# Kernel optimization log

Measured on AMD Instinct MI355X. Metric: run time of the kernel, lower is better.

Reference implementation:

```python
import jax, jax.numpy as jnp
import numpy as np


def setup_inputs() -> dict:
    key = jax.random.key(0)
    k1, k2, k3 = jax.random.split(key, 3)
    B, T, C = 4, 2048, 1024
    x = jax.random.normal(k1, (B, T, C), dtype=jnp.float32)
    # Linear weights stored as (in, out) so y = x @ W + b
    w_attn = jax.random.normal(k2, (C, 3 * C), dtype=jnp.float32) * (1.0 / np.sqrt(C))
    b_attn = jnp.zeros((3 * C,), dtype=jnp.float32)
    w_proj = jax.random.normal(k3, (C, C), dtype=jnp.float32) * (1.0 / np.sqrt(C))
    b_proj = jnp.zeros((C,), dtype=jnp.float32)
    return {"x": x, "w_attn": w_attn, "b_attn": b_attn, "w_proj": w_proj, "b_proj": b_proj}


def reference(x, w_attn, b_attn, w_proj, b_proj):
    B, T, C = x.shape
    n_head = 16
    hd = C // n_head  # head dim = 64
    qkv = x @ w_attn + b_attn  # [B, T, 3C]
    q, k, v = jnp.split(qkv, 3, axis=-1)
    # [B, H, T, hd]
    q = q.reshape(B, T, n_head, hd).transpose(0, 2, 1, 3)
    k = k.reshape(B, T, n_head, hd).transpose(0, 2, 1, 3)
    v = v.reshape(B, T, n_head, hd).transpose(0, 2, 1, 3)
    scale = 1.0 / np.sqrt(hd).astype(np.float32)
    att = jnp.einsum("bhqd,bhkd->bhqk", q, k) * scale  # [B, H, T, T]
    causal = jnp.tril(jnp.ones((T, T), dtype=bool))
    att = jnp.where(causal[None, None], att, jnp.float32(-jnp.inf))
    att = jax.nn.softmax(att, axis=-1)
    y = jnp.einsum("bhqk,bhkd->bhqd", att, v)  # [B, H, T, hd]
    y = y.transpose(0, 2, 1, 3).reshape(B, T, C)
    return y @ w_proj + b_proj
```

## Files before the change

kernel.cpp:

```cpp
#include <hip/hip_runtime.h>

typedef __attribute__((ext_vector_type(8))) short short8;
typedef __attribute__((ext_vector_type(4))) float f32x4;
typedef __attribute__((ext_vector_type(16))) float f32x16;
typedef unsigned short u16;
typedef unsigned int u32;

__device__ __forceinline__ float bf2f(u16 u) {
    union { u32 i; float f; } x;
    x.i = ((u32)u) << 16;
    return x.f;
}

__device__ __forceinline__ u16 f2bf(float f) {
    union { float f; u32 i; } x;
    x.f = f;
    u32 r = x.i + 0x7fffu + ((x.i >> 16) & 1u);
    return (u16)(r >> 16);
}

__device__ __forceinline__ u32 cvt_pk_bf16(float lo, float hi) {
    u32 d;
    asm("v_cvt_pk_bf16_f32 %0, %1, %2" : "=v"(d) : "v"(lo), "v"(hi));
    return d;
}

__device__ __forceinline__ void gload_lds16(const u16* g, u16* l) {
    __builtin_amdgcn_global_load_lds(
        (const __attribute__((address_space(1))) void*)g,
        (__attribute__((address_space(3))) void*)l, 16, 0, 0);
}

__device__ __forceinline__ void pswap(u32& a, u32& b) {
#if __has_builtin(__builtin_amdgcn_permlane32_swap)
    auto r = __builtin_amdgcn_permlane32_swap(a, b, false, false);
    a = r[0];
    b = r[1];
#else
    const int l = (int)(threadIdx.x & 63);
    const u32 ax = __shfl(a, l ^ 32);
    const u32 bx = __shfl(b, l ^ 32);
    a = (l < 32) ? a : bx;
    b = (l < 32) ? ax : b;
#endif
}

#if __has_builtin(__builtin_amdgcn_exp2f)
#define EXP2F(x) __builtin_amdgcn_exp2f(x)
#else
#define EXP2F(x) exp2f(x)
#endif

#define K_SCALE 0.18033688f

__global__ __launch_bounds__(256) void prep_kernel(const float* __restrict__ x,
                                                   u16* __restrict__ xb,
                                                   const float* __restrict__ w_attn,
                                                   u16* __restrict__ wTa) {
    __shared__ float tile[32][33];
    const int tid = threadIdx.x;
    if (blockIdx.x < 4096) {
        const long i = ((long)blockIdx.x * 256 + tid) * 8;
        f32x4 v0 = *(const f32x4*)(x + i);
        f32x4 v1 = *(const f32x4*)(x + i + 4);
        short8 o;
#pragma unroll
        for (int j = 0; j < 4; ++j) o[j] = (short)f2bf(v0[j]);
#pragma unroll
        for (int j = 0; j < 4; ++j) o[4 + j] = (short)f2bf(v1[j]);
        *(short8*)(xb + i) = o;
    } else {
        const int bid = blockIdx.x - 4096;
        const int nb = (bid % 96) * 32, kb = (bid / 96) * 32;
        const int tx = tid & 31, ty = tid >> 5;
#pragma unroll
        for (int i = 0; i < 32; i += 8)
            tile[ty + i][tx] = w_attn[(long)(kb + ty + i) * 3072 + nb + tx];
        __syncthreads();
#pragma unroll
        for (int i = 0; i < 32; i += 8)
            wTa[(long)(nb + ty + i) * 1024 + kb + tx] = f2bf(tile[tx][ty + i]);
    }
}

__global__ __launch_bounds__(256) void transpose_v(const u16* __restrict__ qkv,
                                                   u16* __restrict__ vT) {
    __shared__ u16 tile[32][33];
    const int tb = blockIdx.x * 32;
    const int db = blockIdx.y * 32;
    const int bh = blockIdx.z;
    const int b = bh >> 4, h = bh & 15;
    const int tx = threadIdx.x, ty = threadIdx.y;
#pragma unroll
    for (int i = 0; i < 32; i += 8)
        tile[ty + i][tx] = qkv[((long)b * 2048 + tb + ty + i) * 3072 + 2048 + h * 64 + db + tx];
    __syncthreads();
#pragma unroll
    for (int i = 0; i < 32; i += 8)
        vT[((long)bh * 64 + db + ty + i) * 2048 + tb + tx] = tile[tx][ty + i];
}

#define G1_STAGE(KOFF, SLOT)                                                  \
    gload_lds16(Ag + (KOFF), &As[(SLOT)*4096 + wbase]);                       \
    gload_lds16(Ag + (KOFF) + (long)16 * lda, &As[(SLOT)*4096 + wbase + 512]);\
    gload_lds16(Bg + (KOFF), &Bs[(SLOT)*4096 + wbase]);                       \
    gload_lds16(Bg + (KOFF) + (long)16 * K, &Bs[(SLOT)*4096 + wbase + 512]);

#define G1_COMPUTE(SLOT)                                                      \
    {                                                                         \
        short8 af[4], bf[4];                                                  \
        _Pragma("unroll")                                                     \
        for (int mt = 0; mt < 4; ++mt)                                        \
            af[mt] = *(const short8*)&As[(SLOT)*4096 + (wm + mt*16 + L)*32 + quad*8]; \
        _Pragma("unroll")                                                     \
        for (int nt = 0; nt < 4; ++nt)                                        \
            bf[nt] = *(const short8*)&Bs[(SLOT)*4096 + (wn + nt*16 + L)*32 + quad*8]; \
        _Pragma("unroll")                                                     \
        for (int mt = 0; mt < 4; ++mt)                                        \
            _Pragma("unroll")                                                 \
            for (int nt = 0; nt < 4; ++nt)                                    \
                acc[mt][nt] = __builtin_amdgcn_mfma_f32_16x16x32_bf16(        \
                    af[mt], bf[nt], acc[mt][nt], 0, 0, 0);                    \
    }

__global__ __launch_bounds__(256, 3) void gemm_bf16_bt(
    const u16* __restrict__ A, int lda, const u16* __restrict__ BT,
    const float* __restrict__ bias, u16* __restrict__ C,
    int M, int N, int K) {
    __shared__ __align__(16) u16 As[3 * 128 * 32];
    __shared__ __align__(16) u16 Bs[3 * 128 * 32];
    const int tid = threadIdx.x;
    const int wv = tid >> 6, lane = tid & 63, quad = lane >> 4, L = lane & 15;
    const int wm = (wv >> 1) * 64, wn = (wv & 1) * 64;
    const long m0 = (long)blockIdx.y * 128;
    const long n0 = (long)blockIdx.x * 128;

    const u16* Ag = A + (m0 + wv * 32 + (lane >> 2)) * (long)lda + (lane & 3) * 8;
    const u16* Bg = BT + (n0 + wv * 32 + (lane >> 2)) * (long)K + (lane & 3) * 8;
    const int wbase = wv * 1024;

    f32x4 zero4 = {0.f, 0.f, 0.f, 0.f};
    f32x4 acc[4][4];
#pragma unroll
    for (int i = 0; i < 4; ++i)
#pragma unroll
        for (int j = 0; j < 4; ++j) acc[i][j] = zero4;

    G1_STAGE(0, 0);
    G1_STAGE(32, 1);

    int slot = 0, s2 = 2;
    for (int kb = 0; kb + 64 < K; kb += 32) {
        asm volatile("s_waitcnt vmcnt(4)" ::: "memory");
        __builtin_amdgcn_s_barrier();
        G1_STAGE(kb + 64, s2);
        G1_COMPUTE(slot);
        slot = (slot + 1 == 3) ? 0 : slot + 1;
        s2 = (s2 + 1 == 3) ? 0 : s2 + 1;
    }
    asm volatile("s_waitcnt vmcnt(4)" ::: "memory");
    __builtin_amdgcn_s_barrier();
    G1_COMPUTE(slot);
    slot = (slot + 1 == 3) ? 0 : slot + 1;
    asm volatile("s_waitcnt vmcnt(0)" ::: "memory");
    __builtin_amdgcn_s_barrier();
    G1_COMPUTE(slot);

#pragma unroll
    for (int nt = 0; nt < 4; ++nt) {
        const long col = n0 + wn + nt * 16 + L;
        const float bv = bias[col];
        const float scl = (col >= 1024 && col < 2048) ? K_SCALE : 1.0f;
#pragma unroll
        for (int mt = 0; mt < 4; ++mt)
#pragma unroll
            for (int r = 0; r < 4; ++r) {
                const long row = m0 + wm + mt * 16 + quad * 4 + r;
                C[row * N + col] = f2bf((acc[mt][nt][r] + bv) * scl);
            }
    }
}

__global__ __launch_bounds__(256, 2) void gemm_bf16_bn(
    const u16* __restrict__ A, int lda, const float* __restrict__ B,
    const float* __restrict__ bias, float* __restrict__ C,
    int M, int N, int K) {
    __shared__ __align__(16) u16 As[128 * 32];
    __shared__ __align__(16) u16 Bs[128 * 32];
    const int tid = threadIdx.x;
    const int wv = tid >> 6, lane = tid & 63, quad = lane >> 4, L = lane & 15;
    const int wm = (wv >> 1) * 64, wn = (wv & 1) * 64;
    const long m0 = (long)blockIdx.y * 128;
    const long n0 = (long)blockIdx.x * 128;

    const u16* Ag = A + (m0 + wv * 32 + (lane >> 2)) * (long)lda + (lane & 3) * 8;
    u16* AsW = &As[wv * 32 * 32];

    f32x4 zero4 = {0.f, 0.f, 0.f, 0.f};
    f32x4 acc[4][4];
#pragma unroll
    for (int i = 0; i < 4; ++i)
#pragma unroll
        for (int j = 0; j < 4; ++j) acc[i][j] = zero4;

    for (int kb = 0; kb < K; kb += 32) {
        short8 p[2];
#pragma unroll
        for (int i = 0; i < 2; ++i) {
            const int c = tid + i * 256;
            const int n = c >> 2, k8 = (c & 3) * 8;
            const float* bp = B + (long)(kb + k8) * N + n0 + n;
            float f[8];
#pragma unroll
            for (int j = 0; j < 8; ++j) f[j] = bp[(long)j * N];
            union { u32 d[4]; short8 v; } u;
#pragma unroll
            for (int j = 0; j < 4; ++j) u.d[j] = cvt_pk_bf16(f[2 * j], f[2 * j + 1]);
            p[i] = u.v;
        }
        __syncthreads();
        gload_lds16(Ag + kb, AsW);
        gload_lds16(Ag + kb + (long)16 * lda, AsW + 512);
        *(short8*)(&Bs[tid * 8]) = p[0];
        *(short8*)(&Bs[(tid + 256) * 8]) = p[1];
        __syncthreads();

        short8 af[4], bf[4];
#pragma unroll
        for (int mt = 0; mt < 4; ++mt)
            af[mt] = *(const short8*)&As[(wm + mt * 16 + L) * 32 + quad * 8];
#pragma unroll
        for (int nt = 0; nt < 4; ++nt)
            bf[nt] = *(const short8*)&Bs[(wn + nt * 16 + L) * 32 + quad * 8];
#pragma unroll
        for (int mt = 0; mt < 4; ++mt)
#pragma unroll
            for (int nt = 0; nt < 4; ++nt)
                acc[mt][nt] = __builtin_amdgcn_mfma_f32_16x16x32_bf16(
                    af[mt], bf[nt], acc[mt][nt], 0, 0, 0);
    }

#pragma unroll
    for (int nt = 0; nt < 4; ++nt) {
        const long col = n0 + wn + nt * 16 + L;
        const float bv = bias[col];
#pragma unroll
        for (int mt = 0; mt < 4; ++mt)
#pragma unroll
            for (int r = 0; r < 4; ++r) {
                const long row = m0 + wm + mt * 16 + quad * 4 + r;
                C[row * N + col] = acc[mt][nt][r] + bv;
            }
    }
}

#define AT_T 2048

__global__ __launch_bounds__(256) void attn_kernel(u16* __restrict__ qkv,
                                                   const u16* __restrict__ vT) {
    __shared__ u16 Kt[2][64 * 72];
    __shared__ u16 Vt[2][64 * 72];
    const int tid = threadIdx.x;
    const int wv = tid >> 6, lane = tid & 63;
    const int hi = lane >> 5, cc = lane & 31;
    const int bh = blockIdx.x;
    const int b = bh >> 4, h = bh & 15;
    const long rowbase = (long)b * AT_T;
    const long cbase = (long)h * 64;

    const int srow = tid >> 3, sc = tid & 7;
    const u16* Kg = qkv + (rowbase + srow) * 3072 + 1024 + cbase + sc * 8;
    const u16* Vg = vT + ((long)bh * 64 + srow) * 2048 + sc * 8;
    const int kLo = srow * 72 + sc * 8, kHi = (srow + 32) * 72 + sc * 8;

    short8 ones;
#pragma unroll
    for (int j = 0; j < 8; ++j) ones[j] = (cc == 0) ? (short)0x3F80 : (short)0;

    f32x16 z16;
#pragma unroll
    for (int r = 0; r < 16; ++r) z16[r] = 0.f;

    for (int pass = 0; pass < 2; ++pass) {
        const int qt = (pass == 0) ? (15 - (int)blockIdx.y) : (int)blockIdx.y;
        const int qw = qt * 128 + wv * 32;
        const int nkb = 2 * qt + 2;

        short8 qf[4];
#pragma unroll
        for (int ks = 0; ks < 4; ++ks)
            qf[ks] = *(const short8*)&qkv[(rowbase + qw + cc) * 3072 + cbase + ks * 16 + hi * 8];

        f32x16 accO0, accO1, accL;
#pragma unroll
        for (int r = 0; r < 16; ++r) { accO0[r] = 0.f; accO1[r] = 0.f; accL[r] = 0.f; }

        {
            *(short8*)&Kt[0][kLo] = *(const short8*)Kg;
            *(short8*)&Kt[0][kHi] = *(const short8*)(Kg + (long)32 * 3072);
            *(short8*)&Vt[0][kLo] = *(const short8*)Vg;
            *(short8*)&Vt[0][kHi] = *(const short8*)(Vg + (long)32 * 2048);
        }
        __syncthreads();

        int p = 0;
        for (int kb = 0; kb < nkb; ++kb) {
            const int k0 = kb * 64;
            const bool more = (kb + 1) < nkb;
            short8 kn0, kn1, vn0, vn1;
            if (more) {
                kn0 = *(const short8*)(Kg + (long)(k0 + 64) * 3072);
                kn1 = *(const short8*)(Kg + (long)(k0 + 96) * 3072);
                vn0 = *(const short8*)(Vg + k0 + 64);
                vn1 = *(const short8*)(Vg + (long)32 * 2048 + k0 + 64);
            }

#pragma unroll
            for (int hh = 0; hh < 2; ++hh) {
                const int kh = k0 + 32 * hh;
                if (kh <= qw) {
                    f32x16 s;
                    {
                        short8 kf = *(const short8*)&Kt[p][(32 * hh + cc) * 72 + hi * 8];
                        s = __builtin_amdgcn_mfma_f32_32x32x16_bf16(kf, qf[0], z16, 0, 0, 0);
                    }
#pragma unroll
                    for (int ks = 1; ks < 4; ++ks) {
                        short8 kf = *(const short8*)&Kt[p][(32 * hh + cc) * 72 + ks * 16 + hi * 8];
                        s = __builtin_amdgcn_mfma_f32_32x32x16_bf16(kf, qf[ks], s, 0, 0, 0);
                    }
                    float pe[16];
                    if (kh == qw) {
#pragma unroll
                        for (int r = 0; r < 16; ++r) {
                            const int key = (r & 3) + 8 * (r >> 2) + 4 * hi;
                            const float e = EXP2F(s[r]);
                            pe[r] = (key <= cc) ? e : 0.f;
                        }
                    } else {
#pragma unroll
                        for (int r = 0; r < 16; ++r) pe[r] = EXP2F(s[r]);
                    }

                    short8 pa[2];
#pragma unroll
                    for (int ks = 0; ks < 2; ++ks) {
                        u32 wA = cvt_pk_bf16(pe[8 * ks + 0], pe[8 * ks + 1]);
                        u32 wB = cvt_pk_bf16(pe[8 * ks + 2], pe[8 * ks + 3]);
                        u32 wC = cvt_pk_bf16(pe[8 * ks + 4], pe[8 * ks + 5]);
                        u32 wD = cvt_pk_bf16(pe[8 * ks + 6], pe[8 * ks + 7]);
                        pswap(wA, wC);
                        pswap(wB, wD);
                        union { u32 d[4]; short8 v; } u;
                        u.d[0] = wA; u.d[1] = wB; u.d[2] = wC; u.d[3] = wD;
                        pa[ks] = u.v;
                    }

                    accL = __builtin_amdgcn_mfma_f32_32x32x16_bf16(pa[0], ones, accL, 0, 0, 0);
                    accL = __builtin_amdgcn_mfma_f32_32x32x16_bf16(pa[1], ones, accL, 0, 0, 0);
#pragma unroll
                    for (int ks = 0; ks < 2; ++ks) {
                        short8 vf0 = *(const short8*)&Vt[p][cc * 72 + 32 * hh + ks * 16 + hi * 8];
                        short8 vf1 = *(const short8*)&Vt[p][(32 + cc) * 72 + 32 * hh + ks * 16 + hi * 8];
                        accO0 = __builtin_amdgcn_mfma_f32_32x32x16_bf16(pa[ks], vf0, accO0, 0, 0, 0);
                        accO1 = __builtin_amdgcn_mfma_f32_32x32x16_bf16(pa[ks], vf1, accO1, 0, 0, 0);
                    }
                }
            }

            if (more) {
                *(short8*)&Kt[p ^ 1][kLo] = kn0;
                *(short8*)&Kt[p ^ 1][kHi] = kn1;
                *(short8*)&Vt[p ^ 1][kLo] = vn0;
                *(short8*)&Vt[p ^ 1][kHi] = vn1;
            }
            __syncthreads();
            p ^= 1;
        }

#pragma unroll
        for (int r = 0; r < 16; ++r) {
            const float l = __shfl(accL[r], lane & 32);
            const float inv = 1.f / l;
            const int q = (r & 3) + 8 * (r >> 2) + 4 * hi;
            const long orow = (rowbase + qw + q) * 3072 + cbase;
            qkv[orow + cc] = f2bf(accO0[r] * inv);
            qkv[orow + 32 + cc] = f2bf(accO1[r] * inv);
        }
    }
}

extern "C" void kernel_launch(void* const* d_in, const int* in_sizes, int n_in,
                              void* d_out, int out_size, void* d_ws, size_t ws_size,
                              hipStream_t stream) {
    const float* x      = (const float*)d_in[0];
    const float* w_attn = (const float*)d_in[1];
    const float* b_attn = (const float*)d_in[2];
    const float* w_proj = (const float*)d_in[3];
    const float* b_proj = (const float*)d_in[4];
    float* out = (float*)d_out;

    u16* qkv = (u16*)d_ws;
    u16* xb  = (u16*)d_out;
    u16* wTa = (u16*)((char*)d_out + 16777216);
    u16* vT  = (u16*)d_out;

    prep_kernel<<<4096 + 3072, 256, 0, stream>>>(x, xb, w_attn, wTa);
    gemm_bf16_bt<<<dim3(3072 / 128, 8192 / 128), 256, 0, stream>>>(
        xb, 1024, wTa, b_attn, qkv, 8192, 3072, 1024);
    transpose_v<<<dim3(64, 2, 64), dim3(32, 8), 0, stream>>>(qkv, vT);
    attn_kernel<<<dim3(64, 8), 256, 0, stream>>>(qkv, vT);
    gemm_bf16_bn<<<dim3(1024 / 128, 8192 / 128), 256, 0, stream>>>(
        qkv, 3072, w_proj, b_proj, out, 8192, 1024, 1024);
}
```

Measured before the change: 281.3 us.

## Pre-transpose projection weight to bf16 and reuse pipelined GEMM ring loop

Adds a kernel that transposes and converts w_proj to bf16 into the now-unused V columns of the qkv workspace, so the output projection GEMM can use the same triple-buffered async global-to-LDS ring loop as the QKV GEMM. This replaces per-iteration strided fp32 loads plus conversions and two syncthreads per k-step. It also wraps the attention MFMA sections in s_setprio to favour matrix issue. The cost is one extra small launch, and the design depends on the V region of qkv being dead after the transpose.

After: 252.1 us. 1.12x faster.

```diff
diff --git a/kernel.cpp b/kernel.cpp
--- a/kernel.cpp
+++ b/kernel.cpp
@@ -100,13 +100,27 @@
         vT[((long)bh * 64 + db + ty + i) * 2048 + tb + tx] = tile[tx][ty + i];
 }
 
-#define G1_STAGE(KOFF, SLOT)                                                  \
+__global__ __launch_bounds__(256) void transpose_wp(const float* __restrict__ w,
+                                                    u16* __restrict__ dst) {
+    __shared__ float tile[32][33];
+    const int nb = blockIdx.x * 32, kb = blockIdx.y * 32;
+    const int tx = threadIdx.x & 31, ty = threadIdx.x >> 5;
+#pragma unroll
+    for (int i = 0; i < 32; i += 8)
+        tile[ty + i][tx] = w[(long)(kb + ty + i) * 1024 + nb + tx];
+    __syncthreads();
+#pragma unroll
+    for (int i = 0; i < 32; i += 8)
+        dst[(long)(nb + ty + i) * 3072 + kb + tx] = f2bf(tile[tx][ty + i]);
+}
+
+#define G_STAGE(KOFF, SLOT)                                                   \
     gload_lds16(Ag + (KOFF), &As[(SLOT)*4096 + wbase]);                       \
     gload_lds16(Ag + (KOFF) + (long)16 * lda, &As[(SLOT)*4096 + wbase + 512]);\
     gload_lds16(Bg + (KOFF), &Bs[(SLOT)*4096 + wbase]);                       \
-    gload_lds16(Bg + (KOFF) + (long)16 * K, &Bs[(SLOT)*4096 + wbase + 512]);
-
-#define G1_COMPUTE(SLOT)                                                      \
+    gload_lds16(Bg + (KOFF) + (long)16 * ldbv, &Bs[(SLOT)*4096 + wbase + 512]);
+
+#define G_COMPUTE(SLOT)                                                       \
     {                                                                         \
         short8 af[4], bf[4];                                                  \
         _Pragma("unroll")                                                     \
@@ -123,6 +137,26 @@
                     af[mt], bf[nt], acc[mt][nt], 0, 0, 0);                    \
     }
 
+#define G_RING_LOOP                                                           \
+    G_STAGE(0, 0);                                                            \
+    G_STAGE(32, 1);                                                           \
+    int slot = 0, s2 = 2;                                                     \
+    for (int kb = 0; kb + 64 < K; kb += 32) {                                 \
+        asm volatile("s_waitcnt vmcnt(4)" ::: "memory");                      \
+        __builtin_amdgcn_s_barrier();                                         \
+        G_STAGE(kb + 64, s2);                                                 \
+        G_COMPUTE(slot);                                                      \
+        slot = (slot + 1 == 3) ? 0 : slot + 1;                                \
+        s2 = (s2 + 1 == 3) ? 0 : s2 + 1;                                      \
+    }                                                                         \
+    asm volatile("s_waitcnt vmcnt(4)" ::: "memory");                          \
+    __builtin_amdgcn_s_barrier();                                             \
+    G_COMPUTE(slot);                                                          \
+    slot = (slot + 1 == 3) ? 0 : slot + 1;                                    \
+    asm volatile("s_waitcnt vmcnt(0)" ::: "memory");                          \
+    __builtin_amdgcn_s_barrier();                                             \
+    G_COMPUTE(slot);
+
 __global__ __launch_bounds__(256, 3) void gemm_bf16_bt(
     const u16* __restrict__ A, int lda, const u16* __restrict__ BT,
     const float* __restrict__ bias, u16* __restrict__ C,
@@ -137,6 +171,7 @@
 
     const u16* Ag = A + (m0 + wv * 32 + (lane >> 2)) * (long)lda + (lane & 3) * 8;
     const u16* Bg = BT + (n0 + wv * 32 + (lane >> 2)) * (long)K + (lane & 3) * 8;
+    const long ldbv = K;
     const int wbase = wv * 1024;
 
     f32x4 zero4 = {0.f, 0.f, 0.f, 0.f};
@@ -146,25 +181,7 @@
 #pragma unroll
         for (int j = 0; j < 4; ++j) acc[i][j] = zero4;
 
-    G1_STAGE(0, 0);
-    G1_STAGE(32, 1);
-
-    int slot = 0, s2 = 2;
-    for (int kb = 0; kb + 64 < K; kb += 32) {
-        asm volatile("s_waitcnt vmcnt(4)" ::: "memory");
-        __builtin_amdgcn_s_barrier();
-        G1_STAGE(kb + 64, s2);
-        G1_COMPUTE(slot);
-        slot = (slot + 1 == 3) ? 0 : slot + 1;
-        s2 = (s2 + 1 == 3) ? 0 : s2 + 1;
-    }
-    asm volatile("s_waitcnt vmcnt(4)" ::: "memory");
-    __builtin_amdgcn_s_barrier();
-    G1_COMPUTE(slot);
-    slot = (slot + 1 == 3) ? 0 : slot + 1;
-    asm volatile("s_waitcnt vmcnt(0)" ::: "memory");
-    __builtin_amdgcn_s_barrier();
-    G1_COMPUTE(slot);
+    G_RING_LOOP
 
 #pragma unroll
     for (int nt = 0; nt < 4; ++nt) {
@@ -181,12 +198,12 @@
     }
 }
 
-__global__ __launch_bounds__(256, 2) void gemm_bf16_bn(
-    const u16* __restrict__ A, int lda, const float* __restrict__ B,
+__global__ __launch_bounds__(256, 3) void gemm_bt2(
+    const u16* __restrict__ A, int lda, const u16* __restrict__ BT, int ldb,
     const float* __restrict__ bias, float* __restrict__ C,
     int M, int N, int K) {
-    __shared__ __align__(16) u16 As[128 * 32];
-    __shared__ __align__(16) u16 Bs[128 * 32];
+    __shared__ __align__(16) u16 As[3 * 128 * 32];
+    __shared__ __align__(16) u16 Bs[3 * 128 * 32];
     const int tid = threadIdx.x;
     const int wv = tid >> 6, lane = tid & 63, quad = lane >> 4, L = lane & 15;
     const int wm = (wv >> 1) * 64, wn = (wv & 1) * 64;
@@ -194,7 +211,9 @@
     const long n0 = (long)blockIdx.x * 128;
 
     const u16* Ag = A + (m0 + wv * 32 + (lane >> 2)) * (long)lda + (lane & 3) * 8;
-    u16* AsW = &As[wv * 32 * 32];
+    const u16* Bg = BT + (n0 + wv * 32 + (lane >> 2)) * (long)ldb + (lane & 3) * 8;
+    const long ldbv = ldb;
+    const int wbase = wv * 1024;
 
     f32x4 zero4 = {0.f, 0.f, 0.f, 0.f};
     f32x4 acc[4][4];
@@ -203,42 +222,7 @@
 #pragma unroll
         for (int j = 0; j < 4; ++j) acc[i][j] = zero4;
 
-    for (int kb = 0; kb < K; kb += 32) {
-        short8 p[2];
-#pragma unroll
-        for (int i = 0; i < 2; ++i) {
-            const int c = tid + i * 256;
-            const int n = c >> 2, k8 = (c & 3) * 8;
-            const float* bp = B + (long)(kb + k8) * N + n0 + n;
-            float f[8];
-#pragma unroll
-            for (int j = 0; j < 8; ++j) f[j] = bp[(long)j * N];
-            union { u32 d[4]; short8 v; } u;
-#pragma unroll
-            for (int j = 0; j < 4; ++j) u.d[j] = cvt_pk_bf16(f[2 * j], f[2 * j + 1]);
-            p[i] = u.v;
-        }
-        __syncthreads();
-        gload_lds16(Ag + kb, AsW);
-        gload_lds16(Ag + kb + (long)16 * lda, AsW + 512);
-        *(short8*)(&Bs[tid * 8]) = p[0];
-        *(short8*)(&Bs[(tid + 256) * 8]) = p[1];
-        __syncthreads();
-
-        short8 af[4], bf[4];
-#pragma unroll
-        for (int mt = 0; mt < 4; ++mt)
-            af[mt] = *(const short8*)&As[(wm + mt * 16 + L) * 32 + quad * 8];
-#pragma unroll
-        for (int nt = 0; nt < 4; ++nt)
-            bf[nt] = *(const short8*)&Bs[(wn + nt * 16 + L) * 32 + quad * 8];
-#pragma unroll
-        for (int mt = 0; mt < 4; ++mt)
-#pragma unroll
-            for (int nt = 0; nt < 4; ++nt)
-                acc[mt][nt] = __builtin_amdgcn_mfma_f32_16x16x32_bf16(
-                    af[mt], bf[nt], acc[mt][nt], 0, 0, 0);
-    }
+    G_RING_LOOP
 
 #pragma unroll
     for (int nt = 0; nt < 4; ++nt) {
@@ -320,6 +304,7 @@
                 const int kh = k0 + 32 * hh;
                 if (kh <= qw) {
                     f32x16 s;
+                    __builtin_amdgcn_s_setprio(1);
                     {
                         short8 kf = *(const short8*)&Kt[p][(32 * hh + cc) * 72 + hi * 8];
                         s = __builtin_amdgcn_mfma_f32_32x32x16_bf16(kf, qf[0], z16, 0, 0, 0);
@@ -329,6 +314,7 @@
                         short8 kf = *(const short8*)&Kt[p][(32 * hh + cc) * 72 + ks * 16 + hi * 8];
                         s = __builtin_amdgcn_mfma_f32_32x32x16_bf16(kf, qf[ks], s, 0, 0, 0);
                     }
+                    __builtin_amdgcn_s_setprio(0);
                     float pe[16];
                     if (kh == qw) {
 #pragma unroll
@@ -356,6 +342,7 @@
                         pa[ks] = u.v;
                     }
 
+                    __builtin_amdgcn_s_setprio(1);
                     accL = __builtin_amdgcn_mfma_f32_32x32x16_bf16(pa[0], ones, accL, 0, 0, 0);
                     accL = __builtin_amdgcn_mfma_f32_32x32x16_bf16(pa[1], ones, accL, 0, 0, 0);
 #pragma unroll
@@ -365,6 +352,7 @@
                         accO0 = __builtin_amdgcn_mfma_f32_32x32x16_bf16(pa[ks], vf0, accO0, 0, 0, 0);
                         accO1 = __builtin_amdgcn_mfma_f32_32x32x16_bf16(pa[ks], vf1, accO1, 0, 0, 0);
                     }
+                    __builtin_amdgcn_s_setprio(0);
                 }
             }
 
@@ -404,12 +392,14 @@
     u16* xb  = (u16*)d_out;
     u16* wTa = (u16*)((char*)d_out + 16777216);
     u16* vT  = (u16*)d_out;
+    u16* wTp = qkv + 2048;
 
     prep_kernel<<<4096 + 3072, 256, 0, stream>>>(x, xb, w_attn, wTa);
     gemm_bf16_bt<<<dim3(3072 / 128, 8192 / 128), 256, 0, stream>>>(
         xb, 1024, wTa, b_attn, qkv, 8192, 3072, 1024);
     transpose_v<<<dim3(64, 2, 64), dim3(32, 8), 0, stream>>>(qkv, vT);
+    transpose_wp<<<dim3(32, 32), 256, 0, stream>>>(w_proj, wTp);
     attn_kernel<<<dim3(64, 8), 256, 0, stream>>>(qkv, vT);
-    gemm_bf16_bn<<<dim3(1024 / 128, 8192 / 128), 256, 0, stream>>>(
-        qkv, 3072, w_proj, b_proj, out, 8192, 1024, 1024);
-}
+    gemm_bt2<<<dim3(1024 / 128, 8192 / 128), 256, 0, stream>>>(
+        qkv, 3072, wTp, 3072, b_proj, out, 8192, 1024, 1024);
+}
```
